# Optimization experiments

Hardware: AMD Instinct MI355X
Metric: run time of the kernel (lower is better)

## Reference

```python
import jax, jax.numpy as jnp
import numpy as np
import math

D_MODEL, N_HEADS, D_HEAD = 1024, 16, 64
INIT_RANGE = 0.02
IGNORE = -100000.0


def setup_inputs() -> dict:
    key = jax.random.key(0)
    ks = jax.random.split(key, 5)
    x = jax.random.normal(ks[0], (2, 2048, D_MODEL), dtype=jnp.float32)
    W_Q = INIT_RANGE * jax.random.normal(ks[1], (N_HEADS, D_MODEL, D_HEAD), dtype=jnp.float32)
    W_K = INIT_RANGE * jax.random.normal(ks[2], (N_HEADS, D_MODEL, D_HEAD), dtype=jnp.float32)
    W_V = INIT_RANGE * jax.random.normal(ks[3], (N_HEADS, D_MODEL, D_HEAD), dtype=jnp.float32)
    # W_O is contracted as 'n_heads d_head d_model' in the original einsum
    W_O = INIT_RANGE * jax.random.normal(ks[4], (N_HEADS, D_HEAD, D_MODEL), dtype=jnp.float32)
    b_Q = jnp.zeros((N_HEADS, D_HEAD), dtype=jnp.float32)
    b_K = jnp.zeros((N_HEADS, D_HEAD), dtype=jnp.float32)
    b_V = jnp.zeros((N_HEADS, D_HEAD), dtype=jnp.float32)
    b_O = jnp.zeros((D_MODEL,), dtype=jnp.float32)
    return {"normalized_resid_pre": x, "W_Q": W_Q, "b_Q": b_Q, "W_K": W_K, "b_K": b_K,
            "W_V": W_V, "b_V": b_V, "W_O": W_O, "b_O": b_O}


def reference(normalized_resid_pre, W_Q, b_Q, W_K, b_K, W_V, b_V, W_O, b_O):
    x = normalized_resid_pre  # [b, s, d_model]
    q = jnp.einsum('bsd,hde->bshe', x, W_Q) + b_Q  # [b, s, h, d_head]
    k = jnp.einsum('bsd,hde->bshe', x, W_K) + b_K
    v = jnp.einsum('bsd,hde->bshe', x, W_V) + b_V
    scores = jnp.einsum('bqhe,bkhe->bhqk', q, k) / math.sqrt(D_HEAD)
    S = x.shape[1]
    causal = jnp.tril(jnp.ones((S, S), dtype=bool))  # True where allowed
    scores = jnp.where(causal, scores, IGNORE)
    pattern = jax.nn.softmax(scores, axis=-1)  # [b, h, q, k]
    z = jnp.einsum('bhqk,bkhe->bqhe', pattern, v)
    attn_out = jnp.einsum('bqhe,hed->bqd', z, W_O) + b_O
    return attn_out
```

## Files before the change

kernel.cpp:

```cpp
#include <hip/hip_runtime.h>
#include <cstdint>
#include <cstddef>

typedef unsigned short u16;
typedef __bf16 bf16x8 __attribute__((ext_vector_type(8)));
typedef _Float16 f16x4 __attribute__((ext_vector_type(4)));
typedef _Float16 f16x2 __attribute__((ext_vector_type(2)));
typedef float  f32x4  __attribute__((ext_vector_type(4)));
typedef unsigned short u16x8 __attribute__((ext_vector_type(8)));
typedef unsigned short u16x4 __attribute__((ext_vector_type(4)));

#define DM   1024
#define NH   16
#define DH   64
#define SS   2048
#define BSZ  4096
#define NQKV 3072
#define QSCALE 0.18033688011f

__device__ __forceinline__ u16 f2b(float f) {
  unsigned u = __builtin_bit_cast(unsigned, f);
  return (u16)((u + 0x7FFFu + ((u >> 16) & 1u)) >> 16);
}
__device__ __forceinline__ u16 f2h(float f) {
  _Float16 h = (_Float16)f;
  return __builtin_bit_cast(u16, h);
}

__device__ __forceinline__ void gl_lds16(const void* g, void* l) {
  __builtin_amdgcn_global_load_lds(
      (__attribute__((address_space(1))) void*)(void*)g,
      (__attribute__((address_space(3))) void*)l, 16, 0, 0);
}

__global__ __launch_bounds__(256) void prep_all_kernel(
    const float* __restrict__ x, u16* __restrict__ xb,
    const float* __restrict__ Wq, const float* __restrict__ Wk,
    const float* __restrict__ Wv, u16* __restrict__ wqkvt,
    const float* __restrict__ Wo, u16* __restrict__ wot) {
  __shared__ __align__(16) u16 Ts[64 * 72];
  int bid = blockIdx.x, t = threadIdx.x;
  if (bid < 2048) {
    int i = (bid * 256 + t) * 8;
    float4 a = *(const float4*)(x + i);
    float4 b = *(const float4*)(x + i + 4);
    u16x8 o;
    o[0] = f2b(a.x); o[1] = f2b(a.y); o[2] = f2b(a.z); o[3] = f2b(a.w);
    o[4] = f2b(b.x); o[5] = f2b(b.y); o[6] = f2b(b.z); o[7] = f2b(b.w);
    *(u16x8*)(xb + i) = o;
    return;
  }
  if (bid < 2816) {
    int idx = bid - 2048;
    int dt = idx & 15, sl = idx >> 4;
    int proj = sl >> 4, h = sl & 15;
    const float* W = (proj == 0) ? Wq : ((proj == 1) ? Wk : Wv);
    int d0 = dt * 64;
    {
      int ld = t >> 2;
      int ec = (t & 3) * 16;
      const float* src = W + ((size_t)h * DM + d0 + ld) * DH + ec;
      float4 v0 = *(const float4*)(src);
      float4 v1 = *(const float4*)(src + 4);
      float4 v2 = *(const float4*)(src + 8);
      float4 v3 = *(const float4*)(src + 12);
      float vv[16] = {v0.x, v0.y, v0.z, v0.w, v1.x, v1.y, v1.z, v1.w,
                      v2.x, v2.y, v2.z, v2.w, v3.x, v3.y, v3.z, v3.w};
#pragma unroll
      for (int i = 0; i < 16; i++) Ts[(ec + i) * 72 + ld] = f2b(vv[i]);
    }
    __syncthreads();
    {
      int le = t >> 2;
      int dc = (t & 3) * 16;
      int n = proj * DM + h * DH + le;
      u16* dst = wqkvt + (size_t)n * DM + d0 + dc;
      *(u16x8*)(dst)     = *(const u16x8*)&Ts[le * 72 + dc];
      *(u16x8*)(dst + 8) = *(const u16x8*)&Ts[le * 72 + dc + 8];
    }
    return;
  }
  {
    int idx = bid - 2816;
    int dt = idx & 15, h = idx >> 4;
    int d0 = dt * 64;
    {
      int le = t >> 2;
      int dc = (t & 3) * 16;
      const float* src = Wo + ((size_t)h * DH + le) * DM + d0 + dc;
      float4 v0 = *(const float4*)(src);
      float4 v1 = *(const float4*)(src + 4);
      float4 v2 = *(const float4*)(src + 8);
      float4 v3 = *(const float4*)(src + 12);
      float vv[16] = {v0.x, v0.y, v0.z, v0.w, v1.x, v1.y, v1.z, v1.w,
                      v2.x, v2.y, v2.z, v2.w, v3.x, v3.y, v3.z, v3.w};
#pragma unroll
      for (int i = 0; i < 16; i++) Ts[(dc + i) * 72 + le] = f2b(vv[i]);
    }
    __syncthreads();
    {
      int ld = t >> 2;
      int ec = (t & 3) * 16;
      u16* dst = wot + (size_t)(d0 + ld) * DM + h * DH + ec;
      *(u16x8*)(dst)     = *(const u16x8*)&Ts[ld * 72 + ec];
      *(u16x8*)(dst + 8) = *(const u16x8*)&Ts[ld * 72 + ec + 8];
    }
  }
}

__global__ __launch_bounds__(256) void transpose_v_kernel(const u16* __restrict__ v,
                                                          u16* __restrict__ vt) {
  __shared__ __align__(16) u16 Ts[64 * 72];
  int t = threadIdx.x;
  int st = blockIdx.x;
  int bh = blockIdx.y;
  int s0 = st * 64;
  {
    int ls = t >> 2;
    int ec = (t & 3) * 16;
    const u16* src = v + ((size_t)bh * SS + s0 + ls) * DH + ec;
    u16x8 a0 = *(const u16x8*)src;
    u16x8 a1 = *(const u16x8*)(src + 8);
#pragma unroll
    for (int i = 0; i < 8; i++) Ts[(ec + i) * 72 + ls] = a0[i];
#pragma unroll
    for (int i = 0; i < 8; i++) Ts[(ec + 8 + i) * 72 + ls] = a1[i];
  }
  __syncthreads();
  {
    int le = t >> 2;
    int sc = (t & 3) * 16;
    u16* dst = vt + ((size_t)bh * DH + le) * SS + s0 + sc;
    *(u16x8*)(dst)     = *(const u16x8*)&Ts[le * 72 + sc];
    *(u16x8*)(dst + 8) = *(const u16x8*)&Ts[le * 72 + sc + 8];
  }
}

template <int MODE>
__global__ __launch_bounds__(256) void gemm_bt_kernel(
    const u16* __restrict__ A, const u16* __restrict__ Bt, int K, int N,
    u16* __restrict__ o_q, u16* __restrict__ o_k, u16* __restrict__ o_v,
    const float* __restrict__ c0, const float* __restrict__ c1,
    const float* __restrict__ c2, float* __restrict__ fout) {
  __shared__ __align__(16) u16 As[128 * 32];
  __shared__ __align__(16) u16 Bs[128 * 32];
  int t = threadIdx.x, w = t >> 6, l = t & 63;
  int lr = l & 15, lq = l >> 4;
  int m0 = blockIdx.y * 128, n0 = blockIdx.x * 128;
  int wr = w >> 1, wc = w & 1;
  f32x4 acc[4][4] = {};
  const u16* ga = A + (size_t)(m0 + (t >> 2)) * K + (t & 3) * 8;
  const u16* gb = Bt + (size_t)(n0 + (t >> 2)) * K + (t & 3) * 8;

  for (int k0 = 0; k0 < K; k0 += 32) {
    __syncthreads();
    gl_lds16(ga + k0,           &As[w * 512]);
    gl_lds16(ga + k0 + 64 * K,  &As[2048 + w * 512]);
    gl_lds16(gb + k0,           &Bs[w * 512]);
    gl_lds16(gb + k0 + 64 * K,  &Bs[2048 + w * 512]);
    __syncthreads();
    bf16x8 af[4], bfr[4];
#pragma unroll
    for (int i = 0; i < 4; i++)
      af[i] = *(const bf16x8*)&As[(wr * 64 + i * 16 + lr) * 32 + lq * 8];
#pragma unroll
    for (int j = 0; j < 4; j++)
      bfr[j] = *(const bf16x8*)&Bs[(wc * 64 + j * 16 + lr) * 32 + lq * 8];
#pragma unroll
    for (int i = 0; i < 4; i++)
#pragma unroll
      for (int j = 0; j < 4; j++)
        acc[i][j] = __builtin_amdgcn_mfma_f32_16x16x32_bf16(af[i], bfr[j], acc[i][j], 0, 0, 0);
  }

  int mb = m0 + wr * 64 + lq * 4;
  int nb = n0 + wc * 64 + lr;
  if (MODE == 0) {
#pragma unroll
    for (int j = 0; j < 4; j++) {
      int n = nb + j * 16;
      int proj = n >> 10, r = n & 1023;
      int h = r >> 6, e = r & 63;
      const float* bp = (proj == 0) ? c0 : ((proj == 1) ? c1 : c2);
      float bias = bp[r];
#pragma unroll
      for (int i = 0; i < 4; i++) {
#pragma unroll
        for (int g = 0; g < 4; g++) {
          int m = mb + i * 16 + g;
          int b = m >> 11, s = m & 2047;
          float val = acc[i][j][g] + bias;
          size_t bhh = (size_t)(b * NH + h);
          if (proj == 0)      o_q[(bhh * SS + s) * DH + e] = f2b(val * QSCALE);
          else if (proj == 1) o_k[(bhh * SS + s) * DH + e] = f2b(val);
          else                o_v[(bhh * SS + s) * DH + e] = f2h(val);
        }
      }
    }
  } else {
#pragma unroll
    for (int j = 0; j < 4; j++) {
      int n = nb + j * 16;
      float bias = c0[n];
#pragma unroll
      for (int i = 0; i < 4; i++) {
#pragma unroll
        for (int g = 0; g < 4; g++) {
          int m = mb + i * 16 + g;
          fout[(size_t)m * N + n] = acc[i][j][g] + bias;
        }
      }
    }
  }
}

__global__ __launch_bounds__(256) void attn_kernel(const u16* __restrict__ q_ws,
                                                   const u16* __restrict__ k_ws,
                                                   const u16* __restrict__ vt_ws,
                                                   u16* __restrict__ z_ws) {
  __shared__ __align__(16) u16 Ks[2][64 * 72];
  __shared__ __align__(16) u16 Vs[2][64 * 72];
  int t = threadIdx.x, w = t >> 6, l = t & 63;
  int lr = l & 15, lq = l >> 4;
  int j = blockIdx.x;
  int bh = blockIdx.y;
  const u16* Qb = q_ws + (size_t)bh * SS * DH;
  const u16* Kb = k_ws + (size_t)bh * SS * DH;
  const u16* Vb = vt_ws + (size_t)bh * DH * SS;
  int b = bh >> 4, h = bh & 15;

  int srow = t >> 3;
  int sc8 = (t & 7) * 8;

  for (int half = 0; half < 2; half++) {
    int qt = half ? (31 - j) : j;
    int q0 = qt * 64;
    int nkt = qt + 1;

    int qrow = q0 + w * 16 + lr;
    bf16x8 qf0 = *(const bf16x8*)(Qb + (size_t)qrow * DH + lq * 8);
    bf16x8 qf1 = *(const bf16x8*)(Qb + (size_t)qrow * DH + 32 + lq * 8);

    f32x4 accO[4] = {};
    float mrow = -1e30f, lsum = 0.f;

    __syncthreads();
    {
      const u16* kg = Kb + (size_t)srow * DH + sc8;
      const u16* vg = Vb + (size_t)srow * SS + sc8;
      u16x8 r0 = *(const u16x8*)kg;
      u16x8 r1 = *(const u16x8*)(kg + 32 * DH);
      u16x8 r2 = *(const u16x8*)vg;
      u16x8 r3 = *(const u16x8*)(vg + 32 * SS);
      *(u16x8*)&Ks[0][srow * 72 + sc8] = r0;
      *(u16x8*)&Ks[0][(srow + 32) * 72 + sc8] = r1;
      *(u16x8*)&Vs[0][srow * 72 + sc8] = r2;
      *(u16x8*)&Vs[0][(srow + 32) * 72 + sc8] = r3;
    }

    for (int kt = 0; kt < nkt; ++kt) {
      __syncthreads();
      int pb = kt & 1;

      u16x8 r0, r1, r2, r3;
      bool have_next = (kt + 1 < nkt);
      if (have_next) {
        int k0n = (kt + 1) * 64;
        const u16* kg = Kb + (size_t)(k0n + srow) * DH + sc8;
        const u16* vg = Vb + (size_t)srow * SS + k0n + sc8;
        r0 = *(const u16x8*)kg;
        r1 = *(const u16x8*)(kg + 32 * DH);
        r2 = *(const u16x8*)vg;
        r3 = *(const u16x8*)(vg + 32 * SS);
      }

      f32x4 sc[4];
#pragma unroll
      for (int nt = 0; nt < 4; nt++) {
        bf16x8 kf0 = *(const bf16x8*)&Ks[pb][(nt * 16 + lr) * 72 + lq * 8];
        bf16x8 kf1 = *(const bf16x8*)&Ks[pb][(nt * 16 + lr) * 72 + 32 + lq * 8];
        f32x4 a = {0.f, 0.f, 0.f, 0.f};
        a = __builtin_amdgcn_mfma_f32_16x16x32_bf16(kf0, qf0, a, 0, 0, 0);
        a = __builtin_amdgcn_mfma_f32_16x16x32_bf16(kf1, qf1, a, 0, 0, 0);
        sc[nt] = a;
      }

      if (kt == nkt - 1) {
        int k0 = kt * 64;
        int gq = q0 + w * 16 + lr;
#pragma unroll
        for (int nt = 0; nt < 4; nt++) {
#pragma unroll
          for (int g = 0; g < 4; g++) {
            int gk = k0 + nt * 16 + lq * 4 + g;
            if (gk > gq) sc[nt][g] = -1e30f;
          }
        }
      }

      float mt = -1e30f;
#pragma unroll
      for (int nt = 0; nt < 4; nt++)
#pragma unroll
        for (int g = 0; g < 4; g++) mt = fmaxf(mt, sc[nt][g]);
      mt = fmaxf(mt, __shfl_xor(mt, 16));
      mt = fmaxf(mt, __shfl_xor(mt, 32));

      if (__any(mt > mrow)) {
        float mn = fmaxf(mrow, mt);
        float alpha = exp2f(mrow - mn);
        mrow = mn;
        lsum *= alpha;
#pragma unroll
        for (int et = 0; et < 4; et++)
#pragma unroll
          for (int g = 0; g < 4; g++) accO[et][g] *= alpha;
      }

      f16x4 pf[4];
#pragma unroll
      for (int nt = 0; nt < 4; nt++) {
        float p0 = exp2f(sc[nt][0] - mrow);
        float p1 = exp2f(sc[nt][1] - mrow);
        float p2 = exp2f(sc[nt][2] - mrow);
        float p3 = exp2f(sc[nt][3] - mrow);
        lsum += (p0 + p1) + (p2 + p3);
        f16x2 e0 = __builtin_bit_cast(f16x2, __builtin_amdgcn_cvt_pkrtz(p0, p1));
        f16x2 e1 = __builtin_bit_cast(f16x2, __builtin_amdgcn_cvt_pkrtz(p2, p3));
        pf[nt][0] = e0[0]; pf[nt][1] = e0[1];
        pf[nt][2] = e1[0]; pf[nt][3] = e1[1];
      }

#pragma unroll
      for (int ks = 0; ks < 4; ks++) {
#pragma unroll
        for (int et = 0; et < 4; et++) {
          f16x4 vf = *(const f16x4*)&Vs[pb][(et * 16 + lr) * 72 + ks * 16 + lq * 4];
          accO[et] = __builtin_amdgcn_mfma_f32_16x16x16f16(vf, pf[ks], accO[et], 0, 0, 0);
        }
      }

      if (have_next) {
        int nb2 = (kt + 1) & 1;
        *(u16x8*)&Ks[nb2][srow * 72 + sc8] = r0;
        *(u16x8*)&Ks[nb2][(srow + 32) * 72 + sc8] = r1;
        *(u16x8*)&Vs[nb2][srow * 72 + sc8] = r2;
        *(u16x8*)&Vs[nb2][(srow + 32) * 72 + sc8] = r3;
      }
    }

    lsum += __shfl_xor(lsum, 16);
    lsum += __shfl_xor(lsum, 32);
    float inv = 1.0f / lsum;
    int gq = q0 + w * 16 + lr;
    u16* zrow = z_ws + ((size_t)(b * SS + gq)) * DM + h * DH;
#pragma unroll
    for (int et = 0; et < 4; et++) {
      u16x4 o;
#pragma unroll
      for (int g = 0; g < 4; g++) o[g] = f2b(accO[et][g] * inv);
      *(u16x4*)(zrow + et * 16 + lq * 4) = o;
    }
  }
}

extern "C" void kernel_launch(void* const* d_in, const int* in_sizes, int n_in,
                              void* d_out, int out_size, void* d_ws, size_t ws_size,
                              hipStream_t stream) {
  const float* x  = (const float*)d_in[0];
  const float* Wq = (const float*)d_in[1];
  const float* bq = (const float*)d_in[2];
  const float* Wk = (const float*)d_in[3];
  const float* bk = (const float*)d_in[4];
  const float* Wv = (const float*)d_in[5];
  const float* bv = (const float*)d_in[6];
  const float* Wo = (const float*)d_in[7];
  const float* bo = (const float*)d_in[8];
  float* out = (float*)d_out;

  char* ws = (char*)d_ws;
  const size_t MB = 1u << 20;
  u16* xb    = (u16*)(ws);
  u16* wqkvt = (u16*)(ws + 8 * MB);
  u16* wot   = (u16*)(ws + 14 * MB);
  u16* q_ws  = (u16*)(ws + 16 * MB);
  u16* k_ws  = (u16*)(ws + 24 * MB);
  u16* v_ws  = (u16*)(ws + 32 * MB);
  u16* vt_ws = (u16*)(ws + 40 * MB);
  u16* z_ws  = (u16*)(ws + 48 * MB);

  prep_all_kernel<<<3072, 256, 0, stream>>>(x, xb, Wq, Wk, Wv, wqkvt, Wo, wot);

  gemm_bt_kernel<0><<<dim3(NQKV / 128, BSZ / 128), 256, 0, stream>>>(
      xb, wqkvt, DM, NQKV, q_ws, k_ws, v_ws, bq, bk, bv, nullptr);

  transpose_v_kernel<<<dim3(32, 32), 256, 0, stream>>>(v_ws, vt_ws);

  attn_kernel<<<dim3(16, 32), 256, 0, stream>>>(q_ws, k_ws, vt_ws, z_ws);

  gemm_bt_kernel<1><<<dim3(DM / 128, BSZ / 128), 256, 0, stream>>>(
      z_ws, wot, DM, DM, nullptr, nullptr, nullptr, bo, nullptr, nullptr, out);
}
```

Measured before the change: 218.1 us.

## Split GEMMs, shrink output-projection tile, XCD-aware attention mapping, MFMA row sums

```diff
diff --git a/kernel.cpp b/kernel.cpp
--- a/kernel.cpp
+++ b/kernel.cpp
@@ -136,17 +136,17 @@
   }
 }
 
-template <int MODE>
-__global__ __launch_bounds__(256) void gemm_bt_kernel(
-    const u16* __restrict__ A, const u16* __restrict__ Bt, int K, int N,
+__global__ __launch_bounds__(256) void gemm_qkv_kernel(
+    const u16* __restrict__ A, const u16* __restrict__ Bt,
     u16* __restrict__ o_q, u16* __restrict__ o_k, u16* __restrict__ o_v,
     const float* __restrict__ c0, const float* __restrict__ c1,
-    const float* __restrict__ c2, float* __restrict__ fout) {
+    const float* __restrict__ c2) {
+  const int K = DM;
   __shared__ __align__(16) u16 As[128 * 32];
   __shared__ __align__(16) u16 Bs[128 * 32];
   int t = threadIdx.x, w = t >> 6, l = t & 63;
   int lr = l & 15, lq = l >> 4;
-  int m0 = blockIdx.y * 128, n0 = blockIdx.x * 128;
+  int m0 = blockIdx.x * 128, n0 = blockIdx.y * 128;
   int wr = w >> 1, wc = w & 1;
   f32x4 acc[4][4] = {};
   const u16* ga = A + (size_t)(m0 + (t >> 2)) * K + (t & 3) * 8;
@@ -175,40 +175,74 @@
 
   int mb = m0 + wr * 64 + lq * 4;
   int nb = n0 + wc * 64 + lr;
-  if (MODE == 0) {
-#pragma unroll
-    for (int j = 0; j < 4; j++) {
-      int n = nb + j * 16;
-      int proj = n >> 10, r = n & 1023;
-      int h = r >> 6, e = r & 63;
-      const float* bp = (proj == 0) ? c0 : ((proj == 1) ? c1 : c2);
-      float bias = bp[r];
-#pragma unroll
-      for (int i = 0; i < 4; i++) {
-#pragma unroll
-        for (int g = 0; g < 4; g++) {
-          int m = mb + i * 16 + g;
-          int b = m >> 11, s = m & 2047;
-          float val = acc[i][j][g] + bias;
-          size_t bhh = (size_t)(b * NH + h);
-          if (proj == 0)      o_q[(bhh * SS + s) * DH + e] = f2b(val * QSCALE);
-          else if (proj == 1) o_k[(bhh * SS + s) * DH + e] = f2b(val);
-          else                o_v[(bhh * SS + s) * DH + e] = f2h(val);
-        }
-      }
-    }
-  } else {
-#pragma unroll
-    for (int j = 0; j < 4; j++) {
-      int n = nb + j * 16;
-      float bias = c0[n];
-#pragma unroll
-      for (int i = 0; i < 4; i++) {
-#pragma unroll
-        for (int g = 0; g < 4; g++) {
-          int m = mb + i * 16 + g;
-          fout[(size_t)m * N + n] = acc[i][j][g] + bias;
-        }
+#pragma unroll
+  for (int j = 0; j < 4; j++) {
+    int n = nb + j * 16;
+    int proj = n >> 10, r = n & 1023;
+    int h = r >> 6, e = r & 63;
+    const float* bp = (proj == 0) ? c0 : ((proj == 1) ? c1 : c2);
+    float bias = bp[r];
+#pragma unroll
+    for (int i = 0; i < 4; i++) {
+#pragma unroll
+      for (int g = 0; g < 4; g++) {
+        int m = mb + i * 16 + g;
+        int b = m >> 11, s = m & 2047;
+        float val = acc[i][j][g] + bias;
+        size_t bhh = (size_t)(b * NH + h);
+        if (proj == 0)      o_q[(bhh * SS + s) * DH + e] = f2b(val * QSCALE);
+        else if (proj == 1) o_k[(bhh * SS + s) * DH + e] = f2b(val);
+        else                o_v[(bhh * SS + s) * DH + e] = f2h(val);
+      }
+    }
+  }
+}
+
+__global__ __launch_bounds__(256) void gemm_o_kernel(
+    const u16* __restrict__ A, const u16* __restrict__ Bt,
+    const float* __restrict__ bo, float* __restrict__ fout) {
+  const int K = DM;
+  __shared__ __align__(16) u16 As[128 * 32];
+  __shared__ __align__(16) u16 Bs[64 * 32];
+  int t = threadIdx.x, w = t >> 6, l = t & 63;
+  int lr = l & 15, lq = l >> 4;
+  int m0 = blockIdx.x * 128, n0 = blockIdx.y * 64;
+  f32x4 acc[2][4] = {};
+  const u16* ga = A + (size_t)(m0 + (t >> 2)) * K + (t & 3) * 8;
+  const u16* gb = Bt + (size_t)(n0 + (t >> 2)) * K + (t & 3) * 8;
+
+  for (int k0 = 0; k0 < K; k0 += 32) {
+    __syncthreads();
+    gl_lds16(ga + k0,           &As[w * 512]);
+    gl_lds16(ga + k0 + 64 * K,  &As[2048 + w * 512]);
+    if (t < 256) gl_lds16(gb + k0, &Bs[w * 512]);
+    __syncthreads();
+    bf16x8 af[2], bfr[4];
+#pragma unroll
+    for (int i = 0; i < 2; i++)
+      af[i] = *(const bf16x8*)&As[(w * 32 + i * 16 + lr) * 32 + lq * 8];
+#pragma unroll
+    for (int j = 0; j < 4; j++)
+      bfr[j] = *(const bf16x8*)&Bs[(j * 16 + lr) * 32 + lq * 8];
+#pragma unroll
+    for (int i = 0; i < 2; i++)
+#pragma unroll
+      for (int j = 0; j < 4; j++)
+        acc[i][j] = __builtin_amdgcn_mfma_f32_16x16x32_bf16(af[i], bfr[j], acc[i][j], 0, 0, 0);
+  }
+
+  int mb = m0 + w * 32 + lq * 4;
+  int nb = n0 + lr;
+#pragma unroll
+  for (int j = 0; j < 4; j++) {
+    int n = nb + j * 16;
+    float bias = bo[n];
+#pragma unroll
+    for (int i = 0; i < 2; i++) {
+#pragma unroll
+      for (int g = 0; g < 4; g++) {
+        int m = mb + i * 16 + g;
+        fout[(size_t)m * DM + n] = acc[i][j][g] + bias;
       }
     }
   }
@@ -222,13 +256,17 @@
   __shared__ __align__(16) u16 Vs[2][64 * 72];
   int t = threadIdx.x, w = t >> 6, l = t & 63;
   int lr = l & 15, lq = l >> 4;
-  int j = blockIdx.x;
-  int bh = blockIdx.y;
+  int bid = blockIdx.x;
+  int xcd = bid & 7, idx = bid >> 3;
+  int bh = xcd * 4 + (idx & 3);
+  int j = idx >> 2;
   const u16* Qb = q_ws + (size_t)bh * SS * DH;
   const u16* Kb = k_ws + (size_t)bh * SS * DH;
   const u16* Vb = vt_ws + (size_t)bh * DH * SS;
   int b = bh >> 4, h = bh & 15;
 
+  const f16x4 ones = {(_Float16)1.f, (_Float16)1.f, (_Float16)1.f, (_Float16)1.f};
+
   int srow = t >> 3;
   int sc8 = (t & 7) * 8;
 
@@ -242,7 +280,8 @@
     bf16x8 qf1 = *(const bf16x8*)(Qb + (size_t)qrow * DH + 32 + lq * 8);
 
     f32x4 accO[4] = {};
-    float mrow = -1e30f, lsum = 0.f;
+    f32x4 accL = {};
+    float mrow = -1e30f;
 
     __syncthreads();
     {
@@ -310,7 +349,8 @@
         float mn = fmaxf(mrow, mt);
         float alpha = exp2f(mrow - mn);
         mrow = mn;
-        lsum *= alpha;
+#pragma unroll
+        for (int g = 0; g < 4; g++) accL[g] *= alpha;
 #pragma unroll
         for (int et = 0; et < 4; et++)
 #pragma unroll
@@ -324,7 +364,6 @@
         float p1 = exp2f(sc[nt][1] - mrow);
         float p2 = exp2f(sc[nt][2] - mrow);
         float p3 = exp2f(sc[nt][3] - mrow);
-        lsum += (p0 + p1) + (p2 + p3);
         f16x2 e0 = __builtin_bit_cast(f16x2, __builtin_amdgcn_cvt_pkrtz(p0, p1));
         f16x2 e1 = __builtin_bit_cast(f16x2, __builtin_amdgcn_cvt_pkrtz(p2, p3));
         pf[nt][0] = e0[0]; pf[nt][1] = e0[1];
@@ -333,6 +372,7 @@
 
 #pragma unroll
       for (int ks = 0; ks < 4; ks++) {
+        accL = __builtin_amdgcn_mfma_f32_16x16x16f16(ones, pf[ks], accL, 0, 0, 0);
 #pragma unroll
         for (int et = 0; et < 4; et++) {
           f16x4 vf = *(const f16x4*)&Vs[pb][(et * 16 + lr) * 72 + ks * 16 + lq * 4];
@@ -349,9 +389,7 @@
       }
     }
 
-    lsum += __shfl_xor(lsum, 16);
-    lsum += __shfl_xor(lsum, 32);
-    float inv = 1.0f / lsum;
+    float inv = 1.0f / accL[0];
     int gq = q0 + w * 16 + lr;
     u16* zrow = z_ws + ((size_t)(b * SS + gq)) * DM + h * DH;
 #pragma unroll
@@ -391,13 +429,12 @@
 
   prep_all_kernel<<<3072, 256, 0, stream>>>(x, xb, Wq, Wk, Wv, wqkvt, Wo, wot);
 
-  gemm_bt_kernel<0><<<dim3(NQKV / 128, BSZ / 128), 256, 0, stream>>>(
-      xb, wqkvt, DM, NQKV, q_ws, k_ws, v_ws, bq, bk, bv, nullptr);
+  gemm_qkv_kernel<<<dim3(BSZ / 128, NQKV / 128), 256, 0, stream>>>(
+      xb, wqkvt, q_ws, k_ws, v_ws, bq, bk, bv);
 
   transpose_v_kernel<<<dim3(32, 32), 256, 0, stream>>>(v_ws, vt_ws);
 
-  attn_kernel<<<dim3(16, 32), 256, 0, stream>>>(q_ws, k_ws, vt_ws, z_ws);
-
-  gemm_bt_kernel<1><<<dim3(DM / 128, BSZ / 128), 256, 0, stream>>>(
-      z_ws, wot, DM, DM, nullptr, nullptr, nullptr, bo, nullptr, nullptr, out);
-}
+  attn_kernel<<<512, 256, 0, stream>>>(q_ws, k_ws, vt_ws, z_ws);
+
+  gemm_o_kernel<<<dim3(BSZ / 128, DM / 64), 256, 0, stream>>>(z_ws, wot, bo, out);
+}
```

Result: faster. 201.3 us (-7.7%).
